# Kernel optimization log

Hardware: AMD Instinct MI355X
Metric: run time of the kernel (lower is better)

Reference implementation:

```python
import jax, jax.numpy as jnp
import numpy as np

BATCH = 131072
FEAT = 384
ALPHA = 0.2


def setup_inputs() -> dict:
    key = jax.random.key(0)
    k1, k2, k3 = jax.random.split(key, 3)
    anchor = jax.random.normal(k1, (BATCH, FEAT), dtype=jnp.float32)
    positive = jax.random.normal(k2, (BATCH, FEAT), dtype=jnp.float32)
    negative = jax.random.normal(k3, (BATCH, FEAT), dtype=jnp.float32)
    W = jnp.zeros((FEAT,), dtype=jnp.float32)
    return {"anchor": anchor, "positive": positive, "negative": negative, "W": W}


def reference(anchor, positive, negative, W):
    # A = diag(exp(W)); Mahalanobis distance with diagonal A reduces to
    # an elementwise exp(W)-weighted squared distance (O(N*F), no matmul).
    w = jnp.exp(W)  # [F]
    dp = anchor - positive  # [B, F]
    dn = anchor - negative  # [B, F]
    D_pos = jnp.sum(w * dp * dp, axis=-1)  # [B]
    D_neg = jnp.sum(w * dn * dn, axis=-1)  # [B]
    losses = jax.nn.relu(D_pos - D_neg + jnp.float32(ALPHA))
    return jnp.mean(losses)
```

## Files before the change

kernel.cpp:

```cpp
#include <hip/hip_runtime.h>

constexpr int BATCH = 131072;
constexpr int FEAT  = 384;
constexpr int F4    = FEAT / 4;
constexpr float ALPHA = 0.2f;
constexpr int NBLOCKS = 2048;
constexpr int BLOCK   = 256;
constexpr int WAVES_PER_BLOCK = BLOCK / 64;

__device__ __forceinline__ float wdot(const float4& w, const float4& a,
                                      const float4& p, const float4& n) {
    float dp, dn, r;
    dp = a.x - p.x; dn = a.x - n.x; r  = w.x * (dp * dp - dn * dn);
    dp = a.y - p.y; dn = a.y - n.y; r += w.y * (dp * dp - dn * dn);
    dp = a.z - p.z; dn = a.z - n.z; r += w.z * (dp * dp - dn * dn);
    dp = a.w - p.w; dn = a.w - n.w; r += w.w * (dp * dp - dn * dn);
    return r;
}

__device__ __forceinline__ float wave_sum(float v) {
    #pragma unroll
    for (int m = 1; m < 64; m <<= 1) v += __shfl_xor(v, m, 64);
    return v;
}

__global__ __launch_bounds__(BLOCK) void triplet_partial(
    const float4* __restrict__ A, const float4* __restrict__ P,
    const float4* __restrict__ N, const float* __restrict__ W,
    float* __restrict__ partial)
{
    const int lane = threadIdx.x & 63;
    const int wave = threadIdx.x >> 6;
    const int gw    = blockIdx.x * WAVES_PER_BLOCK + wave;
    const int nwave = gridDim.x * WAVES_PER_BLOCK;

    const float4* W4 = reinterpret_cast<const float4*>(W);
    float4 w0 = W4[lane];
    float4 w1 = W4[(lane < 32) ? (64 + lane) : (lane - 32)];
    float4 w2 = W4[32 + lane];
    w0.x = expf(w0.x); w0.y = expf(w0.y); w0.z = expf(w0.z); w0.w = expf(w0.w);
    w1.x = expf(w1.x); w1.y = expf(w1.y); w1.z = expf(w1.z); w1.w = expf(w1.w);
    w2.x = expf(w2.x); w2.y = expf(w2.y); w2.z = expf(w2.z); w2.w = expf(w2.w);

    float acc = 0.f;
    const int nrp = BATCH / 2;
    for (int rp = gw; rp < nrp; rp += nwave) {
        const int base = rp * (2 * F4);
        float s0, s1;
        {
            const int i = base + lane;
            s0 = wdot(w0, A[i], P[i], N[i]);
        }
        {
            const int i = base + 64 + lane;
            const float v = wdot(w1, A[i], P[i], N[i]);
            if (lane < 32) s0 += v; else s1 = v;
            if (lane < 32) s1 = 0.f;
        }
        {
            const int i = base + 128 + lane;
            s1 += wdot(w2, A[i], P[i], N[i]);
        }
        s0 = wave_sum(s0);
        s1 = wave_sum(s1);
        acc += fmaxf(s0 + ALPHA, 0.f) + fmaxf(s1 + ALPHA, 0.f);
    }

    __shared__ float lds[WAVES_PER_BLOCK];
    if (lane == 0) lds[wave] = acc;
    __syncthreads();
    if (threadIdx.x == 0) {
        float b = 0.f;
        #pragma unroll
        for (int i = 0; i < WAVES_PER_BLOCK; ++i) b += lds[i];
        partial[blockIdx.x] = b;
    }
}

__global__ __launch_bounds__(256) void triplet_finish(
    const float* __restrict__ partial, float* __restrict__ out)
{
    __shared__ float lds[256];
    float s = 0.f;
    for (int i = threadIdx.x; i < NBLOCKS; i += 256) s += partial[i];
    lds[threadIdx.x] = s;
    __syncthreads();
    for (int ofs = 128; ofs > 0; ofs >>= 1) {
        if (threadIdx.x < ofs) lds[threadIdx.x] += lds[threadIdx.x + ofs];
        __syncthreads();
    }
    if (threadIdx.x == 0) out[0] = lds[0] / (float)BATCH;
}

extern "C" void kernel_launch(void* const* d_in, const int* in_sizes, int n_in,
                              void* d_out, int out_size, void* d_ws, size_t ws_size,
                              hipStream_t stream) {
    const float4* A = (const float4*)d_in[0];
    const float4* P = (const float4*)d_in[1];
    const float4* N = (const float4*)d_in[2];
    const float*  W = (const float*)d_in[3];
    float* partial = (float*)d_ws;
    float* out = (float*)d_out;

    triplet_partial<<<NBLOCKS, BLOCK, 0, stream>>>(A, P, N, W, partial);
    triplet_finish<<<1, 256, 0, stream>>>(partial, out);
}
```

Baseline: 111.0 us.

## Double-buffer row tiles in LDS via async global_load_lds

Replaces direct per-wave global loads with a block-level double-buffered pipeline. Each 8-row tile of anchor, positive and negative is copied asynchronously into LDS with global_load_lds while the previous tile is computed, using manual vmcnt waits and barriers. The grid shrinks to 512 blocks that each walk a strided set of tiles. The aim is to keep more memory traffic in flight and hide load latency in this bandwidth-bound reduction. The cost is LDS usage, two barriers per tile, and reliance on hand-written waitcnt values being correct.

```diff
diff --git a/kernel.cpp b/kernel.cpp
--- a/kernel.cpp
+++ b/kernel.cpp
@@ -1,12 +1,18 @@
 #include <hip/hip_runtime.h>
+
+#define AS1 __attribute__((address_space(1)))
+#define AS3 __attribute__((address_space(3)))
 
 constexpr int BATCH = 131072;
 constexpr int FEAT  = 384;
 constexpr int F4    = FEAT / 4;
 constexpr float ALPHA = 0.2f;
-constexpr int NBLOCKS = 2048;
 constexpr int BLOCK   = 256;
-constexpr int WAVES_PER_BLOCK = BLOCK / 64;
+constexpr int NBLOCKS = 512;
+constexpr int ROWS_PER_TILE = 8;
+constexpr int TILE_F4 = ROWS_PER_TILE * F4;
+constexpr int NTILES  = BATCH / ROWS_PER_TILE;
+constexpr int TILES_PER_BLOCK = NTILES / NBLOCKS;
 
 __device__ __forceinline__ float wdot(const float4& w, const float4& a,
                                       const float4& p, const float4& n) {
@@ -18,10 +24,21 @@
     return r;
 }
 
-__device__ __forceinline__ float wave_sum(float v) {
+__device__ __forceinline__ void issue_tile(int wave, int lane,
+    const float4* __restrict__ gA, const float4* __restrict__ gP,
+    const float4* __restrict__ gN,
+    float4* bA, float4* bP, float4* bN)
+{
     #pragma unroll
-    for (int m = 1; m < 64; m <<= 1) v += __shfl_xor(v, m, 64);
-    return v;
+    for (int j = 0; j < 3; ++j) {
+        const int off = 64 * (wave + 4 * j);
+        __builtin_amdgcn_global_load_lds((const AS1 void*)(gA + off + lane),
+                                         (AS3 void*)(bA + off), 16, 0, 0);
+        __builtin_amdgcn_global_load_lds((const AS1 void*)(gP + off + lane),
+                                         (AS3 void*)(bP + off), 16, 0, 0);
+        __builtin_amdgcn_global_load_lds((const AS1 void*)(gN + off + lane),
+                                         (AS3 void*)(bN + off), 16, 0, 0);
+    }
 }
 
 __global__ __launch_bounds__(BLOCK) void triplet_partial(
@@ -29,10 +46,14 @@
     const float4* __restrict__ N, const float* __restrict__ W,
     float* __restrict__ partial)
 {
+    __shared__ float4 sA[2][TILE_F4];
+    __shared__ float4 sP[2][TILE_F4];
+    __shared__ float4 sN[2][TILE_F4];
+    __shared__ float wpart[BLOCK / 64];
+
     const int lane = threadIdx.x & 63;
     const int wave = threadIdx.x >> 6;
-    const int gw    = blockIdx.x * WAVES_PER_BLOCK + wave;
-    const int nwave = gridDim.x * WAVES_PER_BLOCK;
+    const int bid  = blockIdx.x;
 
     const float4* W4 = reinterpret_cast<const float4*>(W);
     float4 w0 = W4[lane];
@@ -41,40 +62,58 @@
     w0.x = expf(w0.x); w0.y = expf(w0.y); w0.z = expf(w0.z); w0.w = expf(w0.w);
     w1.x = expf(w1.x); w1.y = expf(w1.y); w1.z = expf(w1.z); w1.w = expf(w1.w);
     w2.x = expf(w2.x); w2.y = expf(w2.y); w2.z = expf(w2.z); w2.w = expf(w2.w);
+    const bool lo = (lane < 32);
+    const int wbase = 192 * wave;
 
     float acc = 0.f;
-    const int nrp = BATCH / 2;
-    for (int rp = gw; rp < nrp; rp += nwave) {
-        const int base = rp * (2 * F4);
-        float s0, s1;
-        {
-            const int i = base + lane;
-            s0 = wdot(w0, A[i], P[i], N[i]);
+
+    issue_tile(wave, lane, A + (size_t)bid * TILE_F4, P + (size_t)bid * TILE_F4,
+               N + (size_t)bid * TILE_F4, sA[0], sP[0], sN[0]);
+
+    for (int i = 0; i < TILES_PER_BLOCK; ++i) {
+        if (i + 1 < TILES_PER_BLOCK) {
+            const size_t g = (size_t)(bid + NBLOCKS * (i + 1)) * TILE_F4;
+            issue_tile(wave, lane, A + g, P + g, N + g,
+                       sA[(i + 1) & 1], sP[(i + 1) & 1], sN[(i + 1) & 1]);
+            asm volatile("s_waitcnt vmcnt(9)" ::: "memory");
+        } else {
+            asm volatile("s_waitcnt vmcnt(0)" ::: "memory");
         }
-        {
-            const int i = base + 64 + lane;
-            const float v = wdot(w1, A[i], P[i], N[i]);
-            if (lane < 32) s0 += v; else s1 = v;
-            if (lane < 32) s1 = 0.f;
+        __builtin_amdgcn_s_barrier();
+        __builtin_amdgcn_sched_barrier(0);
+
+        const int b = i & 1;
+        const float4 a0 = sA[b][wbase + lane];
+        const float4 p0 = sP[b][wbase + lane];
+        const float4 n0 = sN[b][wbase + lane];
+        const float4 a1 = sA[b][wbase + 64 + lane];
+        const float4 p1 = sP[b][wbase + 64 + lane];
+        const float4 n1 = sN[b][wbase + 64 + lane];
+        const float4 a2 = sA[b][wbase + 128 + lane];
+        const float4 p2 = sP[b][wbase + 128 + lane];
+        const float4 n2 = sN[b][wbase + 128 + lane];
+
+        const float v0 = wdot(w0, a0, p0, n0);
+        const float v1 = wdot(w1, a1, p1, n1);
+        const float v2 = wdot(w2, a2, p2, n2);
+
+        float x0 = v0 + (lo ? v1 : 0.f);
+        float x1 = v2 + (lo ? 0.f : v1);
+        #pragma unroll
+        for (int m = 1; m < 64; m <<= 1) {
+            x0 += __shfl_xor(x0, m, 64);
+            x1 += __shfl_xor(x1, m, 64);
         }
-        {
-            const int i = base + 128 + lane;
-            s1 += wdot(w2, A[i], P[i], N[i]);
-        }
-        s0 = wave_sum(s0);
-        s1 = wave_sum(s1);
-        acc += fmaxf(s0 + ALPHA, 0.f) + fmaxf(s1 + ALPHA, 0.f);
+        acc += fmaxf(x0 + ALPHA, 0.f) + fmaxf(x1 + ALPHA, 0.f);
+
+        __builtin_amdgcn_s_barrier();
+        __builtin_amdgcn_sched_barrier(0);
     }
 
-    __shared__ float lds[WAVES_PER_BLOCK];
-    if (lane == 0) lds[wave] = acc;
+    if (lane == 0) wpart[wave] = acc;
     __syncthreads();
-    if (threadIdx.x == 0) {
-        float b = 0.f;
-        #pragma unroll
-        for (int i = 0; i < WAVES_PER_BLOCK; ++i) b += lds[i];
-        partial[blockIdx.x] = b;
-    }
+    if (threadIdx.x == 0)
+        partial[bid] = wpart[0] + wpart[1] + wpart[2] + wpart[3];
 }
 
 __global__ __launch_bounds__(256) void triplet_finish(
```

Result: faster. 106.7 us (-3.9%).
